# Optimization experiments

Measured on AMD Instinct MI355X. Metric: run time of the kernel, lower is better.

The kernel has to match this reference:

```python
import jax, jax.numpy as jnp
import numpy as np

V, D, H, B, S, T, N_EXTRA = 32000, 256, 512, 16, 400, 100, 50


def _lstm_cell(x, h, c, Wih, Whh, b):
    g = x @ Wih.T + h @ Whh.T + b
    i, f, gg, o = jnp.split(g, 4, axis=-1)
    c = jax.nn.sigmoid(f) * c + jax.nn.sigmoid(i) * jnp.tanh(gg)
    h = jax.nn.sigmoid(o) * jnp.tanh(c)
    return h, c


def _run_lstm(xs, m, Wih, Whh, b):
    # xs: [S,B,D], m: [S,B,1] validity mask (packed-sequence semantics)
    Bz, Hh = xs.shape[1], Whh.shape[1]
    init = (jnp.zeros((Bz, Hh), xs.dtype), jnp.zeros((Bz, Hh), xs.dtype))
    def step(carry, inp):
        h, c = carry
        x, mm = inp
        hn, cn = _lstm_cell(x, h, c, Wih, Whh, b)
        h = jnp.where(mm, hn, h)
        c = jnp.where(mm, cn, c)
        return (h, c), jnp.where(mm, hn, 0.0)
    (h, c), ys = jax.lax.scan(step, init, (xs, m))
    return ys, h, c


def setup_inputs():
    key = jax.random.key(0)
    ks = jax.random.split(key, 20)
    def gn(k, shape, scale=0.05):
        return jax.random.normal(k, shape, dtype=jnp.float32) * scale
    inp = {}
    inp["source"] = jax.random.randint(ks[0], (B, S), 0, V)
    inp["source_extended"] = jax.random.randint(ks[1], (B, S), 0, V + N_EXTRA)
    inp["source_length"] = jax.random.randint(ks[2], (B,), S // 2, S + 1)
    inp["target"] = jax.random.randint(ks[3], (B, T), 0, V)
    inp["emb"] = gn(ks[4], (V, D), 0.1)
    inp["enc_Wih_f"] = gn(ks[5], (4 * H, D))
    inp["enc_Whh_f"] = gn(ks[6], (4 * H, H))
    inp["enc_b_f"] = jnp.zeros((4 * H,), jnp.float32)
    inp["enc_Wih_b"] = gn(ks[7], (4 * H, D))
    inp["enc_Whh_b"] = gn(ks[8], (4 * H, H))
    inp["enc_b_b"] = jnp.zeros((4 * H,), jnp.float32)
    inp["Wproj"] = gn(ks[9], (H, 2 * H))
    inp["bproj"] = jnp.zeros((H,), jnp.float32)
    inp["W2h"] = gn(ks[10], (H, 2 * H))
    inp["b2h"] = jnp.zeros((H,), jnp.float32)
    inp["W2c"] = gn(ks[11], (H, 2 * H))
    inp["b2c"] = jnp.zeros((H,), jnp.float32)
    inp["Wo1"] = gn(ks[12], (H, 2 * H))
    inp["bo1"] = jnp.zeros((H,), jnp.float32)
    inp["Wo2"] = gn(ks[13], (D, H))
    inp["dec_Wih"] = gn(ks[14], (4 * H, 2 * D))
    inp["dec_Whh"] = gn(ks[15], (4 * H, H))
    inp["dec_b"] = jnp.zeros((4 * H,), jnp.float32)
    inp["Wpgen"] = gn(ks[16], (1, 2 * H + 2 * D))
    inp["bpgen"] = jnp.zeros((1,), jnp.float32)
    return inp


def reference(source, source_extended, source_length, target, emb,
              enc_Wih_f, enc_Whh_f, enc_b_f, enc_Wih_b, enc_Whh_b, enc_b_b,
              Wproj, bproj, W2h, b2h, W2c, b2c, Wo1, bo1, Wo2,
              dec_Wih, dec_Whh, dec_b, Wpgen, bpgen):
    mask = jnp.arange(S)[None, :] < source_length[:, None]  # [B,S]
    w_s = emb[source]                                        # [B,S,D]
    xs = jnp.swapaxes(w_s, 0, 1)                             # [S,B,D]
    m = jnp.swapaxes(mask, 0, 1)[:, :, None]                 # [S,B,1]
    # bidirectional LSTM encoder
    ys_f, h_f, c_f = _run_lstm(xs, m, enc_Wih_f, enc_Whh_f, enc_b_f)
    ys_b, h_b, c_b = _run_lstm(xs[::-1], m[::-1], enc_Wih_b, enc_Whh_b, enc_b_b)
    ys_b = ys_b[::-1]
    enc_outs = jnp.swapaxes(jnp.concatenate([ys_f, ys_b], -1), 0, 1)  # [B,S,2H]
    enc_outs = enc_outs @ Wproj.T + bproj                             # [B,S,H]
    dec_h = jnp.concatenate([h_f, h_b], -1) @ W2h.T + b2h             # [B,H]
    dec_c = jnp.concatenate([c_f, c_b], -1) @ W2c.T + b2c             # [B,H]
    lens = source_length[:, None].astype(enc_outs.dtype)
    seq_mean = (enc_outs * mask[..., None]).sum(1) / lens             # [B,H]
    def out_proj(x):
        return jnp.tanh(x @ Wo1.T + bo1) @ Wo2.T
    dec_out0 = out_proj(jnp.concatenate([dec_h, seq_mean], -1))       # [B,D]
    neg = jnp.finfo(enc_outs.dtype).min
    extra = jnp.zeros((B, N_EXTRA), enc_outs.dtype)
    rows = jnp.arange(B)[:, None]
    w_t = jnp.swapaxes(emb[target], 0, 1)                             # [T,B,D]
    def step(carry, x_t):
        dec_out, h, c = carry
        x = jnp.concatenate([x_t, dec_out], -1)                       # [B,2D]
        h, c = _lstm_cell(x, h, c, dec_Wih, dec_Whh, dec_b)
        scores = jnp.einsum('bh,bsh->bs', h, enc_outs)
        attn = jax.nn.softmax(jnp.where(mask, scores, neg), axis=-1)  # point_dist
        context = jnp.einsum('bs,bsh->bh', attn, enc_outs)
        p_gen = jax.nn.sigmoid(jnp.concatenate([context, h, x], -1) @ Wpgen.T + bpgen)  # [B,1]
        dec_out = out_proj(jnp.concatenate([h, context], -1))         # [B,D]
        logit = dec_out @ emb.T                                       # [B,V]
        vocab_dist = jnp.concatenate([p_gen * jax.nn.softmax(logit, axis=-1), extra], -1)
        final = vocab_dist.at[rows, source_extended].add((1.0 - p_gen) * attn) + 1e-20
        return (dec_out, h, c), jnp.log(final)
    _, logits = jax.lax.scan(step, (dec_out0, dec_h, dec_c), w_t)
    return logits  # [T,B,V+N_EXTRA]
```

## Files before the change

### kernel.cpp

```cpp
#include <hip/hip_runtime.h>

#define V_SZ 32000
#define D_SZ 256
#define H_SZ 512
#define B_SZ 16
#define S_SZ 400
#define T_SZ 100
#define G4   2048
#define VX   32050
#define LINE 32

typedef unsigned short ushort_t;
typedef __attribute__((ext_vector_type(8))) __bf16 bf16x8;
typedef __attribute__((ext_vector_type(8))) unsigned short ushort8_t;
typedef __attribute__((ext_vector_type(4))) float f32x4;

__device__ __forceinline__ ushort_t f2bf(float x) {
  union { float f; unsigned u; } v; v.f = x;
  unsigned r = v.u + 0x7fffu + ((v.u >> 16) & 1u);
  return (ushort_t)(r >> 16);
}
__device__ __forceinline__ float bf2f(ushort_t x) {
  union { unsigned u; float f; } v; v.u = ((unsigned)x) << 16; return v.f;
}
__device__ __forceinline__ float bfu2f(unsigned x) {
  union { unsigned u; float f; } v; v.u = x << 16; return v.f;
}
__device__ __forceinline__ float sigf(float x) { return 1.0f / (1.0f + __expf(-x)); }
__device__ __forceinline__ float tanh_f(float x) {
  float e = __expf(2.0f * x);
  return 1.0f - 2.0f / (e + 1.0f);
}
__device__ __forceinline__ float dot4(f32x4 a, f32x4 b) {
  return a.x * b.x + a.y * b.y + a.z * b.z + a.w * b.w;
}
__device__ __forceinline__ void stg(float* p, float v) {
  __hip_atomic_store(p, v, __ATOMIC_RELAXED, __HIP_MEMORY_SCOPE_AGENT);
}
__device__ __forceinline__ void stg_u32(unsigned* p, unsigned v) {
  __hip_atomic_store(p, v, __ATOMIC_RELAXED, __HIP_MEMORY_SCOPE_AGENT);
}

__device__ __forceinline__ void slot_barrier(unsigned* slots, int myslot, int nslots,
                                             unsigned pc) {
  asm volatile("s_waitcnt vmcnt(0)" ::: "memory");
  __syncthreads();
  if (threadIdx.x == 0)
    __hip_atomic_store(&slots[myslot * LINE], pc, __ATOMIC_RELAXED, __HIP_MEMORY_SCOPE_AGENT);
  if (threadIdx.x < 64) {
    const int i0 = threadIdx.x, i1 = threadIdx.x + 64;
    for (;;) {
      unsigned v0 = pc, v1 = pc;
      if (i0 < nslots)
        v0 = __hip_atomic_load(&slots[i0 * LINE], __ATOMIC_RELAXED, __HIP_MEMORY_SCOPE_AGENT);
      if (i1 < nslots)
        v1 = __hip_atomic_load(&slots[i1 * LINE], __ATOMIC_RELAXED, __HIP_MEMORY_SCOPE_AGENT);
      if (__all((v0 >= pc) & (v1 >= pc))) break;
      __builtin_amdgcn_s_sleep(1);
    }
  }
  __syncthreads();
}

__global__ __launch_bounds__(256) void cvt_kernel(const float* in, ushort_t* outp, int n) {
  int i = blockIdx.x * 256 + threadIdx.x;
  int stride = gridDim.x * 256;
  for (; i < n; i += stride) outp[i] = f2bf(in[i]);
}

__global__ __launch_bounds__(256) void cvt_strided_kernel(const float* in, ushort_t* outp) {
  int gid = blockIdx.x * 256 + threadIdx.x;
  int r = gid >> 8, d = gid & 255;
  outp[gid] = f2bf(in[(size_t)r * 512 + d]);
}

__global__ __launch_bounds__(256) void cvt_wo2t_kernel(const float* wo2, ushort_t* outp) {
  int gid = blockIdx.x * 256 + threadIdx.x;
  int h = gid >> 8, d = gid & 255;
  outp[gid] = f2bf(wo2[(size_t)d * 512 + h]);
}

__global__ __launch_bounds__(256) void wfused_kernel(const float* dwih, const float* wo2,
                                                     float* wf) {
  __shared__ float xr_s[256];
  int r = blockIdx.x;
  xr_s[threadIdx.x] = dwih[(size_t)r * 512 + 256 + threadIdx.x];
  __syncthreads();
  float a0 = 0, a1 = 0;
  for (int d = 0; d < 256; ++d) {
    float x = xr_s[d];
    a0 += x * wo2[(size_t)d * 512 + threadIdx.x];
    a1 += x * wo2[(size_t)d * 512 + threadIdx.x + 256];
  }
  wf[(size_t)r * 512 + threadIdx.x] = a0;
  wf[(size_t)r * 512 + threadIdx.x + 256] = a1;
}

__global__ __launch_bounds__(256) void wfp_kernel(const float* wpgen, const float* wo2,
                                                  float* wfp) {
  int h = blockIdx.x * 256 + threadIdx.x;
  float a = 0;
  for (int d = 0; d < 256; ++d) a += wpgen[1280 + d] * wo2[(size_t)d * 512 + h];
  wfp[h] = a;
}

__global__ __launch_bounds__(256) void pack_whh_kernel(const float* whh_f, const float* whh_b,
                                                       ushort_t* outp) {
  int gid = blockIdx.x * 256 + threadIdx.x;
  int col = gid & 511;
  int p_g = gid >> 9;
  int dir = p_g >> 11, p = p_g & 2047;
  int ub = p >> 6, g = (p >> 4) & 3, u = p & 15;
  const float* src = dir ? whh_b : whh_f;
  outp[gid] = f2bf(src[(size_t)(g * 512 + ub * 16 + u) * 512 + col]);
}
// ... 85 lines not shown
  mfma_16x64(ys_cat, wproj_bf, 2 * H_SZ, m0, n0, acc);
  int lane = threadIdx.x & 63, lr = lane & 15, kh = lane >> 4;
#pragma unroll
  for (int s = 0; s < 4; ++s) {
    int n = n0 + s * 16 + lr;
    float bv = bproj[n];
#pragma unroll
    for (int i = 0; i < 4; ++i) {
      int m = m0 + kh * 4 + i;
      int b = m & 15, si = m >> 4;
      enc_outs[((size_t)b * S_SZ + si) * H_SZ + n] = acc[s][i] + bv;
    }
  }
}

__global__ __launch_bounds__(256) void gemm_e2(const ushort_t* emb_bf, const ushort_t* wo2t_bf,
                                               ushort_t* e2) {
  int wave = threadIdx.x >> 6;
  int m0 = blockIdx.y * 16;
  int n0 = blockIdx.x * 256 + wave * 64;
  f32x4 acc[4] = {};
  mfma_16x64(emb_bf, wo2t_bf, 256, m0, n0, acc);
  int lane = threadIdx.x & 63, lr = lane & 15, kh = lane >> 4;
#pragma unroll
  for (int s = 0; s < 4; ++s) {
    int n = n0 + s * 16 + lr;
#pragma unroll
    for (int i = 0; i < 4; ++i) {
      int m = m0 + kh * 4 + i;
      e2[(size_t)m * 512 + n] = f2bf(acc[s][i]);
    }
  }
}

__global__ __launch_bounds__(256) void gemm_logits(const ushort_t* tmp_bf, const ushort_t* e2_bf,
                                                   float* out) {
  int wave = threadIdx.x >> 6;
  int m0 = blockIdx.x * 16;
  int n0 = blockIdx.y * 256 + wave * 64;
  f32x4 acc[4] = {};
  mfma_16x64(tmp_bf, e2_bf, 512, m0, n0, acc);
  int lane = threadIdx.x & 63, lr = lane & 15, kh = lane >> 4;
#pragma unroll
  for (int s = 0; s < 4; ++s) {
    int n = n0 + s * 16 + lr;
#pragma unroll
    for (int i = 0; i < 4; ++i) {
      int m = m0 + kh * 4 + i;
      out[(size_t)m * VX + n] = acc[s][i];
    }
  }
}

__global__ __launch_bounds__(256) void enc_kernel(const float* gx_f, const float* gx_b,
                                                  const ushort_t* whh_pk, const int* src_len,
                                                  unsigned* hbf_f, unsigned* hbf_b,
                                                  unsigned* ys_cat_u32, float* h_final,
                                                  float* c_final, unsigned* ctrs) {
  __shared__ float gates_s[4 * 16 * 17];
  const int blk = blockIdx.x, tid = threadIdx.x;
  const int dir = blk >> 5, ub = blk & 31, j0 = ub * 16;
  const int g = tid >> 6, lane = tid & 63, lr = lane & 15, kh = lane >> 4;
  const float* gx = dir ? gx_b : gx_f;
  unsigned* hb = dir ? hbf_b : hbf_f;
  unsigned* slots = ctrs + dir * 1024;
  const ushort_t* wrow =
      whh_pk + (size_t)(((dir * 32 + ub) * 4 + g) * 16 + lr) * 512 + kh * 8;
  const int bc = tid >> 4, uc = tid & 15;
  const int len_b = src_len[bc];
  float c_reg = 0.0f, h_reg = 0.0f;

  int maxlen;
  {
    int v = src_len[lane & 15];
    v = max(v, __shfl_xor(v, 1));
    v = max(v, __shfl_xor(v, 2));
    v = max(v, __shfl_xor(v, 4));
    v = max(v, __shfl_xor(v, 8));
    maxlen = v;
  }
  for (int i = tid; i < (S_SZ - maxlen) * 128; i += 256) {
    int s = maxlen + (i >> 7);
    int r = i & 127;
    int bb = r >> 3, k = r & 7;
    ys_cat_u32[(size_t)(s * 16 + bb) * 512 + dir * 256 + (j0 >> 1) + k] = 0u;
  }

  float gxa[4];
  {
    const int s0 = dir ? (maxlen - 1) : 0;
    const float* g0 = gx + (size_t)s0 * (16 * 2048) + g * 512 + j0 + lr;
#pragma unroll
    for (int i = 0; i < 4; ++i) gxa[i] = g0[(size_t)(kh * 4 + i) * 2048];
  }

  for (int t = 0; t < maxlen; ++t) {
    const int s_pos = dir ? (maxlen - 1 - t) : t;
    float gxn[4] = {0.f, 0.f, 0.f, 0.f};
    if (t + 1 < maxlen) {
      const int sn = dir ? (maxlen - 2 - t) : (t + 1);
      const float* gn = gx + (size_t)sn * (16 * 2048) + g * 512 + j0 + lr;
#pragma unroll
      for (int i = 0; i < 4; ++i) gxn[i] = gn[(size_t)(kh * 4 + i) * 2048];
    }
    f32x4 acc = {0.f, 0.f, 0.f, 0.f};
    const ushort_t* ap = (const ushort_t*)(hb + (size_t)t * 4096) + lr * 512 + kh * 8;
#pragma unroll
    for (int k0 = 0; k0 < 512; k0 += 32)
      acc = __builtin_amdgcn_mfma_f32_16x16x32_bf16(*(const bf16x8*)(ap + k0),
                                                    *(const bf16x8*)(wrow + k0), acc, 0, 0, 0);
#pragma unroll
    for (int i = 0; i < 4; ++i)
      gates_s[(g * 16 + lr) * 17 + kh * 4 + i] = acc[i] + gxa[i];
    __syncthreads();
    float gi = gates_s[uc * 17 + bc];
    float gf = gates_s[(16 + uc) * 17 + bc];
    float gg = gates_s[(32 + uc) * 17 + bc];
    float go = gates_s[(48 + uc) * 17 + bc];
    bool msk = s_pos < len_b;
    float cn = sigf(gf) * c_reg + sigf(gi) * tanh_f(gg);
    float hn = sigf(go) * tanh_f(cn);
    float hout = msk ? hn : h_reg;
    if (msk) c_reg = cn;
    h_reg = hout;
    unsigned hbits = (unsigned)f2bf(hout);
    unsigned hpart = __shfl_xor(hbits, 1);
    unsigned ybits = msk ? (unsigned)f2bf(hn) : 0u;
    unsigned ypart = __shfl_xor(ybits, 1);
    if ((uc & 1) == 0) {
      stg_u32(&hb[(size_t)(t + 1) * 4096 + bc * 256 + ((j0 + uc) >> 1)], hbits | (hpart << 16));
      ys_cat_u32[(size_t)(s_pos * 16 + bc) * 512 + dir * 256 + ((j0 + uc) >> 1)] =
          ybits | (ypart << 16);
    }
    if (t == maxlen - 1) {
      h_final[dir * 8192 + bc * 512 + j0 + uc] = hout;
      c_final[dir * 8192 + bc * 512 + j0 + uc] = c_reg;
    }
    if (t + 1 < maxlen) slot_barrier(slots, ub, 32, (unsigned)(t + 1));
#pragma unroll
    for (int i = 0; i < 4; ++i) gxa[i] = gxn[i];
  }
}

__global__ __launch_bounds__(256) void seqmean_kernel(const float* enc_outs, const int* src_len,
                                                      float* seq_mean) {
  int b = blockIdx.x >> 1;
  int j = (blockIdx.x & 1) * 256 + threadIdx.x;
  int L = src_len[b];
  float a = 0;
  for (int s = 0; s < L; ++s) a += enc_outs[((size_t)b * S_SZ + s) * H_SZ + j];
  seq_mean[b * 512 + j] = a / (float)L;
}

__global__ __launch_bounds__(256) void init_state_kernel(const float* h_final, const float* c_final,
                                                         const float* w2h, const float* b2h,
                                                         const float* w2c, const float* b2c,
                                                         unsigned* h_u32, float* c_init) {
  int gid = blockIdx.x * 256 + threadIdx.x;
  int half = gid >> 13;
  int idx = gid & 8191;
  int b = idx >> 9, j = idx & 511;
  const float* src = half ? c_final : h_final;
  const float* w = (half ? w2c : w2h) + (size_t)j * 1024;
  float acc = (half ? b2c : b2h)[j];
  const f32x4* s0 = (const f32x4*)(src + b * 512);
  const f32x4* s1 = (const f32x4*)(src + 8192 + b * 512);
  const f32x4* w0 = (const f32x4*)w;
  const f32x4* w1 = w0 + 128;
  float a = 0;
  for (int k = 0; k < 128; ++k) a += dot4(s0[k], w0[k]);
  for (int k = 0; k < 128; ++k) a += dot4(s1[k], w1[k]);
  acc += a;
  if (half) {
    c_init[idx] = acc;
  } else {
    unsigned bits = (unsigned)f2bf(acc);
    unsigned pb2 = __shfl_xor(bits, 1);
    if ((j & 1) == 0) h_u32[b * 256 + (j >> 1)] = bits | (pb2 << 16);
  }
}

__global__ __launch_bounds__(256) void tmp0_kernel(const unsigned* h0_u32, const float* seq_mean,
                                                   const float* wo1, const float* bo1,
                                                   unsigned* tmp_u32) {
  int gid = blockIdx.x * 256 + threadIdx.x;
  int b = gid >> 9, j = gid & 511;
  const f32x4* x1 = (const f32x4*)(seq_mean + b * 512);
  const f32x4* w0 = (const f32x4*)(wo1 + (size_t)j * 1024);
  const f32x4* w1 = w0 + 128;
  float a = bo1[j];
  float p = 0;
  const ushort_t* h0 = (const ushort_t*)(h0_u32) + b * 512;
  for (int k = 0; k < 128; ++k) {
    f32x4 hv = {bf2f(h0[k * 4]), bf2f(h0[k * 4 + 1]), bf2f(h0[k * 4 + 2]), bf2f(h0[k * 4 + 3])};
    p += dot4(hv, w0[k]);
  }
  for (int k = 0; k < 128; ++k) p += dot4(x1[k], w1[k]);
  float tv = tanh_f(a + p);
  unsigned bits = (unsigned)f2bf(tv);
  unsigned pb2 = __shfl_xor(bits, 1);
  if ((j & 1) == 0) tmp_u32[b * 256 + (j >> 1)] = bits | (pb2 << 16);
}

__global__ __launch_bounds__(256) void dec_kernel(
    const ushort_t* xt_bf, const int* src_len, const ushort_t* wdec_pk,
    const float* wpgen, const float* bpgen, const float* wfp, const ushort_t* wo1_bf,
    const float* bo1, const float* enc_outs, const float* gxT, unsigned* h_u32,
    const float* c_init, unsigned* tmp_u32, float* ctx_part, float* z_part, float* zinv,
    float* pgen_o, float* pexp, unsigned* ctrs) {
  __shared__ ushort_t ec_s[50 * 512];
  __shared__ float part_s[4 * 16 * 17];
  __shared__ f32x4 smem4[272];
  __shared__ float red_s[8];
  __shared__ float p_s[64];
  float* sm = (float*)smem4;
  unsigned* gslots = ctrs + 2048;

  const int blk = blockIdx.x, tid = threadIdx.x;
  const int w = tid >> 6, lane = tid & 63, lr = lane & 15, kh = lane >> 4;
  const int j0 = blk * 4;
  const ushort_t* wrow = wdec_pk + (size_t)(blk * 16 + lr) * 1024 + w * 256 + kh * 8;
  const int b_c = (tid >> 2) & 15, u_c = tid & 3;
  float c_reg = (tid < 64) ? c_init[b_c * 512 + j0 + u_c] : 0.0f;
  const int b_pb = blk >> 3, ch = blk & 7, s0c = ch * 50;
  const int len_pb = src_len[b_pb];
  const int nc = ch;
  unsigned* grslots = ctrs + 8192 + b_pb * 256;
  unsigned gpc = 0;

  {
    const f32x4* ebase = (const f32x4*)(enc_outs + ((size_t)b_pb * S_SZ + s0c) * H_SZ);
    unsigned* dst = (unsigned*)ec_s;
    for (int i = tid; i < 6400; i += 256) {
      f32x4 v = ebase[i];
      dst[2 * i] = (unsigned)f2bf(v.x) | ((unsigned)f2bf(v.y) << 16);
      dst[2 * i + 1] = (unsigned)f2bf(v.z) | ((unsigned)f2bf(v.w) << 16);
    }
  }

  float gxa[4] = {0.f, 0.f, 0.f, 0.f};
  if (tid < 64) {
#pragma unroll
    for (int g2 = 0; g2 < 4; ++g2)
      gxa[g2] = gxT[((size_t)(g2 * 512 + j0 + u_c)) * 16 + b_c];
  }

  for (int t = 0; t < T_SZ; ++t) {
    {
      f32x4 acc = {0.f, 0.f, 0.f, 0.f};
      const unsigned* asrc = (w < 2) ? (h_u32 + (size_t)t * 4096) : (tmp_u32 + (size_t)t * 4096);
      const ushort_t* ap = (const ushort_t*)asrc + lr * 512 + (w & 1) * 256 + kh * 8;
#pragma unroll
      for (int k0 = 0; k0 < 256; k0 += 32)
        acc = __builtin_amdgcn_mfma_f32_16x16x32_bf16(*(const bf16x8*)(ap + k0),
                                                      *(const bf16x8*)(wrow + k0), acc, 0, 0, 0);
#pragma unroll
      for (int i = 0; i < 4; ++i) part_s[(w * 16 + lr) * 17 + kh * 4 + i] = acc[i];
      __syncthreads();
      if (tid < 64) {
        float gt[4];
#pragma unroll
        for (int g2 = 0; g2 < 4; ++g2) {
          int p = g2 * 4 + u_c;
          float a = gxa[g2];
#pragma unroll
          for (int w2 = 0; w2 < 4; ++w2) a += part_s[(w2 * 16 + p) * 17 + b_c];
          gt[g2] = a;
        }
        float cn = sigf(gt[1]) * c_reg + sigf(gt[0]) * tanh_f(gt[2]);
        c_reg = cn;
        float hn = sigf(gt[3]) * tanh_f(cn);
        unsigned bits = (unsigned)f2bf(hn);
        unsigned pb2 = __shfl_xor(bits, 1);
        if ((u_c & 1) == 0)
          stg_u32(&h_u32[(size_t)(t + 1) * 4096 + b_c * 256 + ((j0 + u_c) >> 1)],
                  bits | (pb2 << 16));
      }
    }
    slot_barrier(gslots, blk, 128, ++gpc);
    {
      if (tid < 64 && t + 1 < T_SZ) {
#pragma unroll
        for (int g2 = 0; g2 < 4; ++g2)
          gxa[g2] = gxT[((size_t)(t + 1) * G4 + g2 * 512 + j0 + u_c) * 16 + b_c];
      }
      if (tid < 128) {
        unsigned v0 = h_u32[(size_t)(t + 1) * 4096 + b_pb * 256 + tid * 2];
        unsigned v1 = h_u32[(size_t)(t + 1) * 4096 + b_pb * 256 + tid * 2 + 1];
        f32x4 hv = {bfu2f(v0 & 0xffffu), bfu2f(v0 >> 16), bfu2f(v1 & 0xffffu), bfu2f(v1 >> 16)};
        ((f32x4*)sm)[tid] = hv;
      }
      __syncthreads();
      int st = tid >> 2, kq = tid & 3;
      if (st < 50) {
        const ushort8_t* er = (const ushort8_t*)(ec_s + st * 512) + kq * 16;
        const f32x4* hr = (const f32x4*)sm + kq * 32;
        float sc = 0;
#pragma unroll 4
        for (int k = 0; k < 16; ++k) {
          ushort8_t w8 = er[k];
          f32x4 w0 = {bf2f(w8[0]), bf2f(w8[1]), bf2f(w8[2]), bf2f(w8[3])};
          f32x4 w1 = {bf2f(w8[4]), bf2f(w8[5]), bf2f(w8[6]), bf2f(w8[7])};
          sc += dot4(hr[2 * k], w0) + dot4(hr[2 * k + 1], w1);
        }
        sc += __shfl_xor(sc, 1);
        sc += __shfl_xor(sc, 2);
        if (kq == 0) {
          int s_abs = s0c + st;
          float p = (s_abs < len_pb) ? __expf(sc) : 0.0f;
          p_s[st] = p;
          pexp[((size_t)t * 16 + b_pb) * S_SZ + s_abs] = p;
        }
      }
      __syncthreads();
      if (tid == 0) {
        float z = 0;
        for (int s = 0; s < 50; ++s) z += p_s[s];
        stg(&z_part[((size_t)t * 16 + b_pb) * 8 + ch], z);
      }
      float a0 = 0, a1 = 0;
      for (int s = 0; s < 50; ++s) {
        float p = p_s[s];
        a0 += p * bf2f(ec_s[s * 512 + tid]);
        a1 += p * bf2f(ec_s[s * 512 + tid + 256]);
      }
      float* cp = ctx_part + (((size_t)t * 16 + b_pb) * 8 + ch) * 512;
      stg(&cp[tid], a0);
      stg(&cp[tid + 256], a1);
    }
    slot_barrier(grslots, ch, 8, (unsigned)(t + 1));
    {
      float* h_s = sm;
      float* ctx_s = sm + 512;
      const float* zp = z_part + ((size_t)t * 16 + b_pb) * 8;
      float z = 0;
#pragma unroll
      for (int c2 = 0; c2 < 8; ++c2) z += zp[c2];
      float inv = 1.0f / z;
      const float* cpb = ctx_part + ((size_t)t * 16 + b_pb) * 8 * 512;
      float c0 = 0, c1 = 0;
#pragma unroll
      for (int c2 = 0; c2 < 8; ++c2) {
        c0 += cpb[c2 * 512 + tid];
        c1 += cpb[c2 * 512 + tid + 256];
      }
      ctx_s[tid] = c0 * inv;
      ctx_s[tid + 256] = c1 * inv;
      __syncthreads();
      const ushort_t* tmpp = (const ushort_t*)(tmp_u32 + (size_t)t * 4096) + b_pb * 512;
      float tp0 = bf2f(tmpp[tid]);
      float tp1 = bf2f(tmpp[tid + 256]);
      float xe = bf2f(xt_bf[((size_t)t * 16 + b_pb) * 256 + tid]);
      float pg = wpgen[tid] * ctx_s[tid] + wpgen[tid + 256] * ctx_s[tid + 256] +
                 wpgen[512 + tid] * h_s[tid] + wpgen[512 + tid + 256] * h_s[tid + 256] +
                 wpgen[1024 + tid] * xe + wfp[tid] * tp0 + wfp[tid + 256] * tp1;
#pragma unroll
      for (int o = 32; o; o >>= 1) pg += __shfl_xor(pg, o);
      if (lane == 0) red_s[w] = pg;
      __syncthreads();
      if (nc == 0 && tid == 0) {
        pgen_o[t * 16 + b_pb] = sigf(red_s[0] + red_s[1] + red_s[2] + red_s[3] + bpgen[0]);
        zinv[t * 16 + b_pb] = inv;
      }
      int nidx = tid >> 2, kq = tid & 3;
      int n = nc * 64 + nidx;
      const ushort8_t* wrp = (const ushort8_t*)(wo1_bf + (size_t)n * 1024) + kq * 32;
      const f32x4* xr2 =
          (kq < 2) ? ((const f32x4*)h_s + kq * 64) : ((const f32x4*)ctx_s + (kq - 2) * 64);
      float a = 0;
#pragma unroll 4
      for (int k = 0; k < 32; ++k) {
        ushort8_t w8 = wrp[k];
        f32x4 w0 = {bf2f(w8[0]), bf2f(w8[1]), bf2f(w8[2]), bf2f(w8[3])};
        f32x4 w1 = {bf2f(w8[4]), bf2f(w8[5]), bf2f(w8[6]), bf2f(w8[7])};
        a += dot4(xr2[2 * k], w0) + dot4(xr2[2 * k + 1], w1);
      }
      a += __shfl_xor(a, 1);
      a += __shfl_xor(a, 2);
      float tv = tanh_f(a + bo1[n]);
      unsigned bits = (unsigned)f2bf(tv);
      unsigned pbits = __shfl_xor(bits, 4);
      if (kq == 0 && (nidx & 1) == 0)
        stg_u32(&tmp_u32[(size_t)(t + 1) * 4096 + b_pb * 256 + ((nc * 64 + nidx) >> 1)],
                bits | (pbits << 16));
    }
    if (t + 1 < T_SZ) slot_barrier(gslots, blk, 128, ++gpc);
  }
}

__global__ __launch_bounds__(1024) void finalize_kernel(float* out, const float* pexp,
                                                        const float* zinv, const float* pgen_i,
                                                        const int* src_ext) {
  __shared__ float scat[VX];
  __shared__ float red[64];
  const int row = blockIdx.x;
  const int b = row & 15;
  const int tid = threadIdx.x;
  for (int i = tid; i < VX; i += 1024) scat[i] = 0.0f;
  __syncthreads();
  const float pg = pgen_i[row];
  const float inv = zinv[row];
  if (tid < S_SZ) {
    float v = (1.0f - pg) * pexp[(size_t)row * S_SZ + tid] * inv;
    int col = src_ext[b * S_SZ + tid];
    atomicAdd(&scat[col], v);
  }
  float* orow = out + (size_t)row * VX;
  float l[32];
  float mx = -3.4e38f;
#pragma unroll
  for (int i2 = 0; i2 < 32; ++i2) {
    int col = tid + (i2 << 10);
    l[i2] = (col < V_SZ) ? orow[col] : -3.4e38f;
    mx = fmaxf(mx, l[i2]);
  }
#pragma unroll
  for (int o = 32; o; o >>= 1) mx = fmaxf(mx, __shfl_xor(mx, o));
  if ((tid & 63) == 0) red[16 + (tid >> 6)] = mx;
  __syncthreads();
  if (tid == 0) {
    float m2 = red[16];
    for (int w = 1; w < 16; ++w) m2 = fmaxf(m2, red[16 + w]);
    red[0] = m2;
  }
  __syncthreads();
  const float gmx = red[0];
  float se = 0.0f;
#pragma unroll
  for (int i2 = 0; i2 < 32; ++i2) {
    int col = tid + (i2 << 10);
    if (col < V_SZ) {
      l[i2] = __expf(l[i2] - gmx);
      se += l[i2];
    }
  }
#pragma unroll
  for (int o = 32; o; o >>= 1) se += __shfl_xor(se, o);
  if ((tid & 63) == 0) red[32 + (tid >> 6)] = se;
  __syncthreads();
// ... 1 lines not shown
    float s2 = 0;
    for (int w = 0; w < 16; ++w) s2 += red[32 + w];
    red[1] = s2;
  }
  __syncthreads();
  const float scale = pg / red[1];
#pragma unroll
  for (int i2 = 0; i2 < 32; ++i2) {
    int col = tid + (i2 << 10);
    if (col < VX) {
      float base = (col < V_SZ) ? l[i2] * scale : 0.0f;
      orow[col] = __logf(base + scat[col] + 1e-20f);
    }
  }
}

extern "C" void kernel_launch(void* const* d_in, const int* in_sizes, int n_in, void* d_out,
                              int out_size, void* d_ws, size_t ws_size, hipStream_t stream) {
  (void)in_sizes; (void)n_in; (void)out_size; (void)ws_size;
  const int* source = (const int*)d_in[0];
  const int* source_ext = (const int*)d_in[1];
  const int* source_len = (const int*)d_in[2];
  const int* target = (const int*)d_in[3];
  const float* emb = (const float*)d_in[4];
  const float* wih_f = (const float*)d_in[5];
  const float* whh_f = (const float*)d_in[6];
  const float* b_f = (const float*)d_in[7];
  const float* wih_b = (const float*)d_in[8];
  const float* whh_b = (const float*)d_in[9];
  const float* b_b = (const float*)d_in[10];
  const float* wproj = (const float*)d_in[11];
  const float* bproj = (const float*)d_in[12];
  const float* w2h = (const float*)d_in[13];
  const float* b2h = (const float*)d_in[14];
  const float* w2c = (const float*)d_in[15];
  const float* b2c = (const float*)d_in[16];
  const float* wo1 = (const float*)d_in[17];
  const float* bo1 = (const float*)d_in[18];
  const float* wo2 = (const float*)d_in[19];
  const float* dwih = (const float*)d_in[20];
  const float* dwhh = (const float*)d_in[21];
  const float* dbias = (const float*)d_in[22];
  const float* wpgen = (const float*)d_in[23];
  const float* bpgen = (const float*)d_in[24];
  float* out = (float*)d_out;

  size_t off = 0;
  char* wsb = (char*)d_ws;
  auto alloc = [&](size_t bytes) -> void* {
    void* p = wsb + off;
    off += (bytes + 255) & ~(size_t)255;
    return p;
  };
  unsigned* ctrs = (unsigned*)alloc(64 * 1024);
  ushort_t* emb_bf = (ushort_t*)alloc((size_t)V_SZ * D_SZ * 2);
  ushort_t* wihf_bf = (ushort_t*)alloc((size_t)G4 * D_SZ * 2);
  ushort_t* wihb_bf = (ushort_t*)alloc((size_t)G4 * D_SZ * 2);
  ushort_t* wihd_bf = (ushort_t*)alloc((size_t)G4 * D_SZ * 2);
  ushort_t* wproj_bf = (ushort_t*)alloc((size_t)H_SZ * 2 * H_SZ * 2);
  ushort_t* wo2t_bf = (ushort_t*)alloc((size_t)H_SZ * D_SZ * 2);
  ushort_t* wo1_bf = (ushort_t*)alloc((size_t)H_SZ * 1024 * 2);
  float* wfused = (float*)alloc((size_t)G4 * H_SZ * 4);
  float* wfp = (float*)alloc(512 * 4);
  ushort_t* whh_pk = (ushort_t*)alloc((size_t)2 * G4 * H_SZ * 2);
  ushort_t* wdec_pk = (ushort_t*)alloc((size_t)G4 * 1024 * 2);
  ushort_t* xs_bf = (ushort_t*)alloc((size_t)S_SZ * B_SZ * D_SZ * 2);
  ushort_t* xt_bf = (ushort_t*)alloc((size_t)T_SZ * B_SZ * D_SZ * 2);
  float* gx_f = (float*)alloc((size_t)S_SZ * B_SZ * G4 * 4);
  float* gx_b = (float*)alloc((size_t)S_SZ * B_SZ * G4 * 4);
  unsigned* hbf_f = (unsigned*)alloc((size_t)(S_SZ + 1) * 4096 * 4);
  unsigned* hbf_b = (unsigned*)alloc((size_t)(S_SZ + 1) * 4096 * 4);
  unsigned* ys_cat_u32 = (unsigned*)alloc((size_t)S_SZ * B_SZ * 512 * 4);
  float* h_final = (float*)alloc((size_t)2 * B_SZ * H_SZ * 4);
  float* c_final = (float*)alloc((size_t)2 * B_SZ * H_SZ * 4);
  float* enc_outs = (float*)alloc((size_t)B_SZ * S_SZ * H_SZ * 4);
  float* seq_mean = (float*)alloc((size_t)B_SZ * H_SZ * 4);
  unsigned* h_u32 = (unsigned*)alloc((size_t)(T_SZ + 1) * 4096 * 4);
  float* c_init = (float*)alloc((size_t)B_SZ * H_SZ * 4);
  unsigned* tmp_u32 = (unsigned*)alloc((size_t)(T_SZ + 1) * 4096 * 4);
  float* z_part = (float*)alloc((size_t)T_SZ * B_SZ * 8 * 4);
  float* zinv = (float*)alloc((size_t)T_SZ * B_SZ * 4);
  float* pgen_b = (float*)alloc((size_t)T_SZ * B_SZ * 4);
  float* pexp = (float*)alloc((size_t)T_SZ * B_SZ * S_SZ * 4);
  ushort_t* e2_bf = (ushort_t*)gx_f;
  float* gx_dec = gx_b;
  float* ctx_part = gx_b + (size_t)3276800;
  float* gxT = gx_b + (size_t)9830400;

  hipMemsetAsync(ctrs, 0, 64 * 1024, stream);
  hipMemsetAsync(hbf_f, 0, 4096 * 4, stream);
  hipMemsetAsync(hbf_b, 0, 4096 * 4, stream);

  cvt_kernel<<<2048, 256, 0, stream>>>(emb, emb_bf, V_SZ * D_SZ);
  cvt_kernel<<<2048, 256, 0, stream>>>(wih_f, wihf_bf, G4 * D_SZ);
  cvt_kernel<<<2048, 256, 0, stream>>>(wih_b, wihb_bf, G4 * D_SZ);
  cvt_kernel<<<2048, 256, 0, stream>>>(wproj, wproj_bf, H_SZ * 2 * H_SZ);
  cvt_kernel<<<2048, 256, 0, stream>>>(wo1, wo1_bf, H_SZ * 1024);
  cvt_strided_kernel<<<2048, 256, 0, stream>>>(dwih, wihd_bf);
  cvt_wo2t_kernel<<<512, 256, 0, stream>>>(wo2, wo2t_bf);
  wfused_kernel<<<2048, 256, 0, stream>>>(dwih, wo2, wfused);
  wfp_kernel<<<2, 256, 0, stream>>>(wpgen, wo2, wfp);
  pack_whh_kernel<<<8192, 256, 0, stream>>>(whh_f, whh_b, whh_pk);
  pack_wdec_kernel<<<8192, 256, 0, stream>>>(dwhh, wfused, wdec_pk);
  gather_src_kernel<<<800, 256, 0, stream>>>(emb_bf, source, xs_bf);
  gather_tgt_kernel<<<200, 256, 0, stream>>>(emb_bf, target, xt_bf);
  gemm_abt_bias<<<dim3(8, 400), 256, 0, stream>>>(xs_bf, wihf_bf, b_f, gx_f, 256);
  gemm_abt_bias<<<dim3(8, 400), 256, 0, stream>>>(xs_bf, wihb_bf, b_b, gx_b, 256);
  enc_kernel<<<64, 256, 0, stream>>>(gx_f, gx_b, whh_pk, source_len, hbf_f, hbf_b, ys_cat_u32,
                                     h_final, c_final, ctrs);
  gemm_encout<<<dim3(2, 400), 256, 0, stream>>>((const ushort_t*)ys_cat_u32, wproj_bf, bproj,
                                                enc_outs);
  seqmean_kernel<<<32, 256, 0, stream>>>(enc_outs, source_len, seq_mean);
  init_state_kernel<<<64, 256, 0, stream>>>(h_final, c_final, w2h, b2h, w2c, b2c, h_u32, c_init);
  tmp0_kernel<<<32, 256, 0, stream>>>(h_u32, seq_mean, wo1, bo1, tmp_u32);
  gemm_abt_bias<<<dim3(8, 100), 256, 0, stream>>>(xt_bf, wihd_bf, dbias, gx_dec, 256);
  gxT_kernel<<<dim3(8, 100), 256, 0, stream>>>(gx_dec, gxT);
  gemm_e2<<<dim3(2, 2000), 256, 0, stream>>>(emb_bf, wo2t_bf, e2_bf);
  dec_kernel<<<128, 256, 0, stream>>>(xt_bf, source_len, wdec_pk, wpgen, bpgen, wfp, wo1_bf, bo1,
                                      enc_outs, gxT, h_u32, c_init, tmp_u32, ctx_part, z_part,
                                      zinv, pgen_b, pexp, ctrs);
  gemm_logits<<<dim3(100, 125), 256, 0, stream>>>((const ushort_t*)(tmp_u32 + 4096), e2_bf, out);
  finalize_kernel<<<1600, 1024, 0, stream>>>(out, pexp, zinv, pgen_b, source_ext);
}
```

Before: 4.863 ms.

## Replace counter-slot grid barriers with sentinel-valued data polling in recurrent kernels

```diff
diff --git a/kernel.cpp b/kernel.cpp
--- a/kernel.cpp
+++ b/kernel.cpp
@@ -8,7 +8,7 @@
 #define T_SZ 100
 #define G4   2048
 #define VX   32050
-#define LINE 32
+#define SENTU 0xFFFFFFFFu
 
 typedef unsigned short ushort_t;
 typedef __attribute__((ext_vector_type(8))) __bf16 bf16x8;
@@ -26,6 +26,9 @@
 __device__ __forceinline__ float bfu2f(unsigned x) {
   union { unsigned u; float f; } v; v.u = x << 16; return v.f;
 }
+__device__ __forceinline__ float u2f(unsigned x) {
+  union { unsigned u; float f; } v; v.u = x; return v.f;
+}
 __device__ __forceinline__ float sigf(float x) { return 1.0f / (1.0f + __expf(-x)); }
 __device__ __forceinline__ float tanh_f(float x) {
   float e = __expf(2.0f * x);
@@ -40,27 +43,11 @@
 __device__ __forceinline__ void stg_u32(unsigned* p, unsigned v) {
   __hip_atomic_store(p, v, __ATOMIC_RELAXED, __HIP_MEMORY_SCOPE_AGENT);
 }
-
-__device__ __forceinline__ void slot_barrier(unsigned* slots, int myslot, int nslots,
-                                             unsigned pc) {
-  asm volatile("s_waitcnt vmcnt(0)" ::: "memory");
-  __syncthreads();
-  if (threadIdx.x == 0)
-    __hip_atomic_store(&slots[myslot * LINE], pc, __ATOMIC_RELAXED, __HIP_MEMORY_SCOPE_AGENT);
-  if (threadIdx.x < 64) {
-    const int i0 = threadIdx.x, i1 = threadIdx.x + 64;
-    for (;;) {
-      unsigned v0 = pc, v1 = pc;
-      if (i0 < nslots)
-        v0 = __hip_atomic_load(&slots[i0 * LINE], __ATOMIC_RELAXED, __HIP_MEMORY_SCOPE_AGENT);
-      if (i1 < nslots)
-        v1 = __hip_atomic_load(&slots[i1 * LINE], __ATOMIC_RELAXED, __HIP_MEMORY_SCOPE_AGENT);
-      if (__all((v0 >= pc) & (v1 >= pc))) break;
-      __builtin_amdgcn_s_sleep(1);
-    }
-  }
-  __syncthreads();
-}
+__device__ __forceinline__ unsigned pollu(const unsigned* p) {
+  return __hip_atomic_load(p, __ATOMIC_RELAXED, __HIP_MEMORY_SCOPE_AGENT);
+}
+
+union U8 { unsigned u[4]; bf16x8 v; };
 
 __global__ __launch_bounds__(256) void cvt_kernel(const float* in, ushort_t* outp, int n) {
   int i = blockIdx.x * 256 + threadIdx.x;
@@ -256,19 +243,22 @@
                                                   const ushort_t* whh_pk, const int* src_len,
                                                   unsigned* hbf_f, unsigned* hbf_b,
                                                   unsigned* ys_cat_u32, float* h_final,
-                                                  float* c_final, unsigned* ctrs) {
+                                                  float* c_final) {
   __shared__ float gates_s[4 * 16 * 17];
   const int blk = blockIdx.x, tid = threadIdx.x;
   const int dir = blk >> 5, ub = blk & 31, j0 = ub * 16;
   const int g = tid >> 6, lane = tid & 63, lr = lane & 15, kh = lane >> 4;
   const float* gx = dir ? gx_b : gx_f;
   unsigned* hb = dir ? hbf_b : hbf_f;
-  unsigned* slots = ctrs + dir * 1024;
   const ushort_t* wrow =
       whh_pk + (size_t)(((dir * 32 + ub) * 4 + g) * 16 + lr) * 512 + kh * 8;
   const int bc = tid >> 4, uc = tid & 15;
   const int len_b = src_len[bc];
   float c_reg = 0.0f, h_reg = 0.0f;
+
+  bf16x8 wv[16];
+#pragma unroll
+  for (int k = 0; k < 16; ++k) wv[k] = *(const bf16x8*)(wrow + k * 32);
 
   int maxlen;
   {
@@ -303,12 +293,33 @@
 #pragma unroll
       for (int i = 0; i < 4; ++i) gxn[i] = gn[(size_t)(kh * 4 + i) * 2048];
     }
+    U8 hv[16];
+    if (t == 0) {
+#pragma unroll
+      for (int k = 0; k < 16; ++k) {
+        hv[k].u[0] = 0; hv[k].u[1] = 0; hv[k].u[2] = 0; hv[k].u[3] = 0;
+      }
+    } else {
+      const unsigned* hp = hb + (size_t)t * 4096 + lr * 256 + kh * 4;
+      for (;;) {
+        unsigned okm = 1u;
+#pragma unroll
+        for (int k = 0; k < 16; ++k) {
+#pragma unroll
+          for (int q = 0; q < 4; ++q) {
+            unsigned v = pollu(&hp[k * 16 + q]);
+            hv[k].u[q] = v;
+            okm &= (v != SENTU) ? 1u : 0u;
+          }
+        }
+        if (__all((int)okm)) break;
+        __builtin_amdgcn_s_sleep(1);
+      }
+    }
     f32x4 acc = {0.f, 0.f, 0.f, 0.f};
-    const ushort_t* ap = (const ushort_t*)(hb + (size_t)t * 4096) + lr * 512 + kh * 8;
-#pragma unroll
-    for (int k0 = 0; k0 < 512; k0 += 32)
-      acc = __builtin_amdgcn_mfma_f32_16x16x32_bf16(*(const bf16x8*)(ap + k0),
-                                                    *(const bf16x8*)(wrow + k0), acc, 0, 0, 0);
+#pragma unroll
+    for (int k = 0; k < 16; ++k)
+      acc = __builtin_amdgcn_mfma_f32_16x16x32_bf16(hv[k].v, wv[k], acc, 0, 0, 0);
 #pragma unroll
     for (int i = 0; i < 4; ++i)
       gates_s[(g * 16 + lr) * 17 + kh * 4 + i] = acc[i] + gxa[i];
@@ -336,7 +347,7 @@
       h_final[dir * 8192 + bc * 512 + j0 + uc] = hout;
       c_final[dir * 8192 + bc * 512 + j0 + uc] = c_reg;
     }
-    if (t + 1 < maxlen) slot_barrier(slots, ub, 32, (unsigned)(t + 1));
+    __syncthreads();
 #pragma unroll
     for (int i = 0; i < 4; ++i) gxa[i] = gxn[i];
   }
@@ -407,14 +418,13 @@
     const float* wpgen, const float* bpgen, const float* wfp, const ushort_t* wo1_bf,
     const float* bo1, const float* enc_outs, const float* gxT, unsigned* h_u32,
     const float* c_init, unsigned* tmp_u32, float* ctx_part, float* z_part, float* zinv,
-    float* pgen_o, float* pexp, unsigned* ctrs) {
+    float* pgen_o, float* pexp) {
   __shared__ ushort_t ec_s[50 * 512];
   __shared__ float part_s[4 * 16 * 17];
   __shared__ f32x4 smem4[272];
   __shared__ float red_s[8];
   __shared__ float p_s[64];
   float* sm = (float*)smem4;
-  unsigned* gslots = ctrs + 2048;
 
   const int blk = blockIdx.x, tid = threadIdx.x;
   const int w = tid >> 6, lane = tid & 63, lr = lane & 15, kh = lane >> 4;
@@ -425,8 +435,10 @@
   const int b_pb = blk >> 3, ch = blk & 7, s0c = ch * 50;
   const int len_pb = src_len[b_pb];
   const int nc = ch;
-  unsigned* grslots = ctrs + 8192 + b_pb * 256;
-  unsigned gpc = 0;
+
+  bf16x8 wv[8];
+#pragma unroll
+  for (int k = 0; k < 8; ++k) wv[k] = *(const bf16x8*)(wrow + k * 32);
 
   {
     const f32x4* ebase = (const f32x4*)(enc_outs + ((size_t)b_pb * S_SZ + s0c) * H_SZ);
@@ -447,13 +459,27 @@
 
   for (int t = 0; t < T_SZ; ++t) {
     {
+      const unsigned* asrc = (w < 2) ? (h_u32 + (size_t)t * 4096) : (tmp_u32 + (size_t)t * 4096);
+      const unsigned* hp = asrc + lr * 256 + (w & 1) * 128 + kh * 4;
+      U8 hv[8];
+      for (;;) {
+        unsigned okm = 1u;
+#pragma unroll
+        for (int k = 0; k < 8; ++k) {
+#pragma unroll
+          for (int q = 0; q < 4; ++q) {
+            unsigned v = pollu(&hp[k * 16 + q]);
+            hv[k].u[q] = v;
+            okm &= (v != SENTU) ? 1u : 0u;
+          }
+        }
+        if (__all((int)okm)) break;
+        __builtin_amdgcn_s_sleep(1);
+      }
       f32x4 acc = {0.f, 0.f, 0.f, 0.f};
-      const unsigned* asrc = (w < 2) ? (h_u32 + (size_t)t * 4096) : (tmp_u32 + (size_t)t * 4096);
-      const ushort_t* ap = (const ushort_t*)asrc + lr * 512 + (w & 1) * 256 + kh * 8;
-#pragma unroll
-      for (int k0 = 0; k0 < 256; k0 += 32)
-        acc = __builtin_amdgcn_mfma_f32_16x16x32_bf16(*(const bf16x8*)(ap + k0),
-                                                      *(const bf16x8*)(wrow + k0), acc, 0, 0, 0);
+#pragma unroll
+      for (int k = 0; k < 8; ++k)
+        acc = __builtin_amdgcn_mfma_f32_16x16x32_bf16(hv[k].v, wv[k], acc, 0, 0, 0);
 #pragma unroll
       for (int i = 0; i < 4; ++i) part_s[(w * 16 + lr) * 17 + kh * 4 + i] = acc[i];
       __syncthreads();
@@ -476,8 +502,8 @@
           stg_u32(&h_u32[(size_t)(t + 1) * 4096 + b_c * 256 + ((j0 + u_c) >> 1)],
                   bits | (pb2 << 16));
       }
-    }
-    slot_barrier(gslots, blk, 128, ++gpc);
+      __syncthreads();
+    }
     {
       if (tid < 64 && t + 1 < T_SZ) {
 #pragma unroll
@@ -485,8 +511,14 @@
           gxa[g2] = gxT[((size_t)(t + 1) * G4 + g2 * 512 + j0 + u_c) * 16 + b_c];
       }
       if (tid < 128) {
-        unsigned v0 = h_u32[(size_t)(t + 1) * 4096 + b_pb * 256 + tid * 2];
-        unsigned v1 = h_u32[(size_t)(t + 1) * 4096 + b_pb * 256 + tid * 2 + 1];
+        const unsigned* hp = h_u32 + (size_t)(t + 1) * 4096 + b_pb * 256 + tid * 2;
+        unsigned v0, v1;
+        for (;;) {
+          v0 = pollu(hp);
+          v1 = pollu(hp + 1);
+          if (__all((v0 != SENTU) & (v1 != SENTU))) break;
+          __builtin_amdgcn_s_sleep(1);
+        }
         f32x4 hv = {bfu2f(v0 & 0xffffu), bfu2f(v0 >> 16), bfu2f(v1 & 0xffffu), bfu2f(v1 >> 16)};
         ((f32x4*)sm)[tid] = hv;
       }
@@ -528,28 +560,46 @@
       stg(&cp[tid], a0);
       stg(&cp[tid + 256], a1);
     }
-    slot_barrier(grslots, ch, 8, (unsigned)(t + 1));
     {
       float* h_s = sm;
       float* ctx_s = sm + 512;
-      const float* zp = z_part + ((size_t)t * 16 + b_pb) * 8;
+      const unsigned* zpu = (const unsigned*)(z_part + ((size_t)t * 16 + b_pb) * 8);
+      const unsigned* cpu = (const unsigned*)(ctx_part + ((size_t)t * 16 + b_pb) * 8 * 512);
+      const unsigned* tpu = tmp_u32 + (size_t)t * 4096 + b_pb * 256;
+      unsigned zv[8], cva[8], cvb[8], tva, tvb;
+      for (;;) {
+        unsigned okm = 1u;
+#pragma unroll
+        for (int c2 = 0; c2 < 8; ++c2) {
+          zv[c2] = pollu(&zpu[c2]);
+          okm &= (zv[c2] != SENTU) ? 1u : 0u;
+          cva[c2] = pollu(&cpu[c2 * 512 + tid]);
+          okm &= (cva[c2] != SENTU) ? 1u : 0u;
+          cvb[c2] = pollu(&cpu[c2 * 512 + tid + 256]);
+          okm &= (cvb[c2] != SENTU) ? 1u : 0u;
+        }
+        tva = pollu(&tpu[tid >> 1]);
+        okm &= (tva != SENTU) ? 1u : 0u;
+        tvb = pollu(&tpu[128 + (tid >> 1)]);
+        okm &= (tvb != SENTU) ? 1u : 0u;
+        if (__all((int)okm)) break;
+        __builtin_amdgcn_s_sleep(1);
+      }
       float z = 0;
 #pragma unroll
-      for (int c2 = 0; c2 < 8; ++c2) z += zp[c2];
+      for (int c2 = 0; c2 < 8; ++c2) z += u2f(zv[c2]);
       float inv = 1.0f / z;
-      const float* cpb = ctx_part + ((size_t)t * 16 + b_pb) * 8 * 512;
       float c0 = 0, c1 = 0;
 #pragma unroll
       for (int c2 = 0; c2 < 8; ++c2) {
-        c0 += cpb[c2 * 512 + tid];
-        c1 += cpb[c2 * 512 + tid + 256];
+        c0 += u2f(cva[c2]);
+        c1 += u2f(cvb[c2]);
       }
       ctx_s[tid] = c0 * inv;
       ctx_s[tid + 256] = c1 * inv;
       __syncthreads();
-      const ushort_t* tmpp = (const ushort_t*)(tmp_u32 + (size_t)t * 4096) + b_pb * 512;
-      float tp0 = bf2f(tmpp[tid]);
-      float tp1 = bf2f(tmpp[tid + 256]);
+      float tp0 = bf2f((ushort_t)((tid & 1) ? (tva >> 16) : (tva & 0xffffu)));
+      float tp1 = bf2f((ushort_t)((tid & 1) ? (tvb >> 16) : (tvb & 0xffffu)));
       float xe = bf2f(xt_bf[((size_t)t * 16 + b_pb) * 256 + tid]);
       float pg = wpgen[tid] * ctx_s[tid] + wpgen[tid + 256] * ctx_s[tid + 256] +
                  wpgen[512 + tid] * h_s[tid] + wpgen[512 + tid + 256] * h_s[tid + 256] +
@@ -583,8 +633,8 @@
       if (kq == 0 && (nidx & 1) == 0)
         stg_u32(&tmp_u32[(size_t)(t + 1) * 4096 + b_pb * 256 + ((nc * 64 + nidx) >> 1)],
                 bits | (pbits << 16));
-    }
-    if (t + 1 < T_SZ) slot_barrier(gslots, blk, 128, ++gpc);
+      __syncthreads();
+    }
   }
 }
 
@@ -692,7 +742,6 @@
     off += (bytes + 255) & ~(size_t)255;
     return p;
   };
-  unsigned* ctrs = (unsigned*)alloc(64 * 1024);
   ushort_t* emb_bf = (ushort_t*)alloc((size_t)V_SZ * D_SZ * 2);
   ushort_t* wihf_bf = (ushort_t*)alloc((size_t)G4 * D_SZ * 2);
   ushort_t* wihb_bf = (ushort_t*)alloc((size_t)G4 * D_SZ * 2);
@@ -727,9 +776,11 @@
   float* ctx_part = gx_b + (size_t)3276800;
   float* gxT = gx_b + (size_t)9830400;
 
-  hipMemsetAsync(ctrs, 0, 64 * 1024, stream);
-  hipMemsetAsync(hbf_f, 0, 4096 * 4, stream);
-  hipMemsetAsync(hbf_b, 0, 4096 * 4, stream);
+  hipMemsetAsync(hbf_f, 0xFF, (size_t)(S_SZ + 1) * 4096 * 4, stream);
+  hipMemsetAsync(hbf_b, 0xFF, (size_t)(S_SZ + 1) * 4096 * 4, stream);
+  hipMemsetAsync(h_u32, 0xFF, (size_t)(T_SZ + 1) * 4096 * 4, stream);
+  hipMemsetAsync(tmp_u32, 0xFF, (size_t)(T_SZ + 1) * 4096 * 4, stream);
+  hipMemsetAsync(z_part, 0xFF, (size_t)T_SZ * B_SZ * 8 * 4, stream);
 
   cvt_kernel<<<2048, 256, 0, stream>>>(emb, emb_bf, V_SZ * D_SZ);
   cvt_kernel<<<2048, 256, 0, stream>>>(wih_f, wihf_bf, G4 * D_SZ);
@@ -747,7 +798,7 @@
   gemm_abt_bias<<<dim3(8, 400), 256, 0, stream>>>(xs_bf, wihf_bf, b_f, gx_f, 256);
   gemm_abt_bias<<<dim3(8, 400), 256, 0, stream>>>(xs_bf, wihb_bf, b_b, gx_b, 256);
   enc_kernel<<<64, 256, 0, stream>>>(gx_f, gx_b, whh_pk, source_len, hbf_f, hbf_b, ys_cat_u32,
-                                     h_final, c_final, ctrs);
+                                     h_final, c_final);
   gemm_encout<<<dim3(2, 400), 256, 0, stream>>>((const ushort_t*)ys_cat_u32, wproj_bf, bproj,
                                                 enc_outs);
   seqmean_kernel<<<32, 256, 0, stream>>>(enc_outs, source_len, seq_mean);
@@ -756,9 +807,10 @@
   gemm_abt_bias<<<dim3(8, 100), 256, 0, stream>>>(xt_bf, wihd_bf, dbias, gx_dec, 256);
   gxT_kernel<<<dim3(8, 100), 256, 0, stream>>>(gx_dec, gxT);
   gemm_e2<<<dim3(2, 2000), 256, 0, stream>>>(emb_bf, wo2t_bf, e2_bf);
+  hipMemsetAsync(ctx_part, 0xFF, (size_t)T_SZ * B_SZ * 8 * H_SZ * 4, stream);
   dec_kernel<<<128, 256, 0, stream>>>(xt_bf, source_len, wdec_pk, wpgen, bpgen, wfp, wo1_bf, bo1,
                                       enc_outs, gxT, h_u32, c_init, tmp_u32, ctx_part, z_part,
-                                      zinv, pgen_b, pexp, ctrs);
+                                      zinv, pgen_b, pexp);
   gemm_logits<<<dim3(100, 125), 256, 0, stream>>>((const ushort_t*)(tmp_u32 + 4096), e2_bf, out);
   finalize_kernel<<<1600, 1024, 0, stream>>>(out, pexp, zinv, pgen_b, source_ext);
 }
```

Result: slower. 7.452 ms (+53.2%).

## Pin encoder LSTM blocks to one XCC per direction and sync via local L2

Applied to the files above, without the earlier changes.

```diff
diff --git a/kernel.cpp b/kernel.cpp
--- a/kernel.cpp
+++ b/kernel.cpp
@@ -39,6 +39,20 @@
 }
 __device__ __forceinline__ void stg_u32(unsigned* p, unsigned v) {
   __hip_atomic_store(p, v, __ATOMIC_RELAXED, __HIP_MEMORY_SCOPE_AGENT);
+}
+__device__ __forceinline__ unsigned pollu(const unsigned* p) {
+  return __hip_atomic_load(p, __ATOMIC_RELAXED, __HIP_MEMORY_SCOPE_AGENT);
+}
+__device__ __forceinline__ unsigned ld_sc0(const unsigned* p) {
+  unsigned v;
+  asm volatile("global_load_dword %0, %1, off sc0\n\ts_waitcnt vmcnt(0)"
+               : "=&v"(v) : "v"(p) : "memory");
+  return v;
+}
+__device__ __forceinline__ int xcc_id() {
+  unsigned v;
+  asm volatile("s_getreg_b32 %0, hwreg(HW_REG_XCC_ID)" : "=s"(v));
+  return (int)(v & 0xf);
 }
 
 __device__ __forceinline__ void slot_barrier(unsigned* slots, int myslot, int nslots,
@@ -252,23 +266,45 @@
   }
 }
 
-__global__ __launch_bounds__(256) void enc_kernel(const float* gx_f, const float* gx_b,
-                                                  const ushort_t* whh_pk, const int* src_len,
-                                                  unsigned* hbf_f, unsigned* hbf_b,
-                                                  unsigned* ys_cat_u32, float* h_final,
-                                                  float* c_final, unsigned* ctrs) {
-  __shared__ float gates_s[4 * 16 * 17];
-  const int blk = blockIdx.x, tid = threadIdx.x;
-  const int dir = blk >> 5, ub = blk & 31, j0 = ub * 16;
+__global__ __launch_bounds__(256, 1) void enc_kernel(const float* gx_f, const float* gx_b,
+                                                     const ushort_t* whh_pk, const int* src_len,
+                                                     unsigned* hb_f, unsigned* hb_b,
+                                                     unsigned* hbM_f, unsigned* hbM_b,
+                                                     unsigned* ys_cat_u32, float* h_final,
+                                                     float* c_final, unsigned* ctrs) {
+  __shared__ float big_s[25600];
+  __shared__ int role_s;
+  __shared__ int ok_s;
+  float* gates_s = big_s;
+  const int tid = threadIdx.x;
+  if (tid == 0) {
+    int xcc = xcc_id();
+    int r = -1;
+    if (xcc == 0) {
+      unsigned i = atomicAdd(&ctrs[12288], 1u);
+      if (i < 32u) r = (int)i;
+    } else if (xcc == 1) {
+      unsigned i = atomicAdd(&ctrs[12320], 1u);
+      if (i < 32u) r = 32 + (int)i;
+    }
+    role_s = r;
+  }
+  __syncthreads();
+  const int role = role_s;
+  if (role < 0) return;
+  const int dir = role >> 5, ub = role & 31, j0 = ub * 16;
   const int g = tid >> 6, lane = tid & 63, lr = lane & 15, kh = lane >> 4;
   const float* gx = dir ? gx_b : gx_f;
-  unsigned* hb = dir ? hbf_b : hbf_f;
-  unsigned* slots = ctrs + dir * 1024;
+  unsigned* hb = dir ? hb_b : hb_f;
+  unsigned* hbM = dir ? hbM_b : hbM_f;
+  unsigned* tl = ctrs + dir * 1024;
+  unsigned* tm = ctrs + 2048 + dir * 1024;
   const ushort_t* wrow =
       whh_pk + (size_t)(((dir * 32 + ub) * 4 + g) * 16 + lr) * 512 + kh * 8;
   const int bc = tid >> 4, uc = tid & 15;
   const int len_b = src_len[bc];
   float c_reg = 0.0f, h_reg = 0.0f;
+  bool slow = false;
 
   int maxlen;
   {
@@ -281,8 +317,8 @@
   }
   for (int i = tid; i < (S_SZ - maxlen) * 128; i += 256) {
     int s = maxlen + (i >> 7);
-    int r = i & 127;
-    int bb = r >> 3, k = r & 7;
+    int r2 = i & 127;
+    int bb = r2 >> 3, k = r2 & 7;
     ys_cat_u32[(size_t)(s * 16 + bb) * 512 + dir * 256 + (j0 >> 1) + k] = 0u;
   }
 
@@ -303,8 +339,34 @@
 #pragma unroll
       for (int i = 0; i < 4; ++i) gxn[i] = gn[(size_t)(kh * 4 + i) * 2048];
     }
+    const unsigned* hsrcbuf = hb;
+    if (t > 0) {
+      if (tid < 64) {
+        int ok = 0;
+        if (!slow) {
+          for (int it = 0; it < 2000; ++it) {
+            unsigned v = (unsigned)t;
+            if (lane < 32) v = ld_sc0(&tl[lane * 32]);
+            if (__all((int)(v >= (unsigned)t))) { ok = 1; break; }
+            __builtin_amdgcn_s_sleep(1);
+          }
+        }
+        if (!ok) {
+          for (;;) {
+            unsigned v = (unsigned)t;
+            if (lane < 32) v = pollu(&tm[lane * 32]);
+            if (__all((int)(v >= (unsigned)t))) break;
+            __builtin_amdgcn_s_sleep(1);
+          }
+        }
+        if (tid == 0) ok_s = ok;
+      }
+      __syncthreads();
+      if (!ok_s) slow = true;
+      hsrcbuf = ok_s ? hb : hbM;
+    }
     f32x4 acc = {0.f, 0.f, 0.f, 0.f};
-    const ushort_t* ap = (const ushort_t*)(hb + (size_t)t * 4096) + lr * 512 + kh * 8;
+    const ushort_t* ap = (const ushort_t*)(hsrcbuf + (size_t)t * 4096) + lr * 512 + kh * 8;
 #pragma unroll
     for (int k0 = 0; k0 < 512; k0 += 32)
       acc = __builtin_amdgcn_mfma_f32_16x16x32_bf16(*(const bf16x8*)(ap + k0),
@@ -328,7 +390,10 @@
     unsigned ybits = msk ? (unsigned)f2bf(hn) : 0u;
     unsigned ypart = __shfl_xor(ybits, 1);
     if ((uc & 1) == 0) {
-      stg_u32(&hb[(size_t)(t + 1) * 4096 + bc * 256 + ((j0 + uc) >> 1)], hbits | (hpart << 16));
+      unsigned wv2 = hbits | (hpart << 16);
+      size_t ix = (size_t)(t + 1) * 4096 + bc * 256 + ((j0 + uc) >> 1);
+      hb[ix] = wv2;
+      stg_u32(&hbM[ix], wv2);
       ys_cat_u32[(size_t)(s_pos * 16 + bc) * 512 + dir * 256 + ((j0 + uc) >> 1)] =
           ybits | (ypart << 16);
     }
@@ -336,7 +401,12 @@
       h_final[dir * 8192 + bc * 512 + j0 + uc] = hout;
       c_final[dir * 8192 + bc * 512 + j0 + uc] = c_reg;
     }
-    if (t + 1 < maxlen) slot_barrier(slots, ub, 32, (unsigned)(t + 1));
+    asm volatile("s_waitcnt vmcnt(0)" ::: "memory");
+    __syncthreads();
+    if (tid == 0) {
+      tl[ub * 32] = (unsigned)(t + 1);
+      stg_u32(&tm[ub * 32], (unsigned)(t + 1));
+    }
 #pragma unroll
     for (int i = 0; i < 4; ++i) gxa[i] = gxn[i];
   }
@@ -414,7 +484,7 @@
   __shared__ float red_s[8];
   __shared__ float p_s[64];
   float* sm = (float*)smem4;
-  unsigned* gslots = ctrs + 2048;
+  unsigned* gslots = ctrs + 4096;
 
   const int blk = blockIdx.x, tid = threadIdx.x;
   const int w = tid >> 6, lane = tid & 63, lr = lane & 15, kh = lane >> 4;
@@ -708,8 +778,10 @@
   ushort_t* xt_bf = (ushort_t*)alloc((size_t)T_SZ * B_SZ * D_SZ * 2);
   float* gx_f = (float*)alloc((size_t)S_SZ * B_SZ * G4 * 4);
   float* gx_b = (float*)alloc((size_t)S_SZ * B_SZ * G4 * 4);
-  unsigned* hbf_f = (unsigned*)alloc((size_t)(S_SZ + 1) * 4096 * 4);
-  unsigned* hbf_b = (unsigned*)alloc((size_t)(S_SZ + 1) * 4096 * 4);
+  unsigned* hb_f = (unsigned*)alloc((size_t)(S_SZ + 1) * 4096 * 4);
+  unsigned* hb_b = (unsigned*)alloc((size_t)(S_SZ + 1) * 4096 * 4);
+  unsigned* hbM_f = (unsigned*)alloc((size_t)(S_SZ + 1) * 4096 * 4);
+  unsigned* hbM_b = (unsigned*)alloc((size_t)(S_SZ + 1) * 4096 * 4);
   unsigned* ys_cat_u32 = (unsigned*)alloc((size_t)S_SZ * B_SZ * 512 * 4);
   float* h_final = (float*)alloc((size_t)2 * B_SZ * H_SZ * 4);
   float* c_final = (float*)alloc((size_t)2 * B_SZ * H_SZ * 4);
@@ -728,8 +800,10 @@
   float* gxT = gx_b + (size_t)9830400;
 
   hipMemsetAsync(ctrs, 0, 64 * 1024, stream);
-  hipMemsetAsync(hbf_f, 0, 4096 * 4, stream);
-  hipMemsetAsync(hbf_b, 0, 4096 * 4, stream);
+  hipMemsetAsync(hb_f, 0, 4096 * 4, stream);
+  hipMemsetAsync(hb_b, 0, 4096 * 4, stream);
+  hipMemsetAsync(hbM_f, 0, 4096 * 4, stream);
+  hipMemsetAsync(hbM_b, 0, 4096 * 4, stream);
 
   cvt_kernel<<<2048, 256, 0, stream>>>(emb, emb_bf, V_SZ * D_SZ);
   cvt_kernel<<<2048, 256, 0, stream>>>(wih_f, wihf_bf, G4 * D_SZ);
@@ -746,8 +820,8 @@
   gather_tgt_kernel<<<200, 256, 0, stream>>>(emb_bf, target, xt_bf);
   gemm_abt_bias<<<dim3(8, 400), 256, 0, stream>>>(xs_bf, wihf_bf, b_f, gx_f, 256);
   gemm_abt_bias<<<dim3(8, 400), 256, 0, stream>>>(xs_bf, wihb_bf, b_b, gx_b, 256);
-  enc_kernel<<<64, 256, 0, stream>>>(gx_f, gx_b, whh_pk, source_len, hbf_f, hbf_b, ys_cat_u32,
-                                     h_final, c_final, ctrs);
+  enc_kernel<<<256, 256, 0, stream>>>(gx_f, gx_b, whh_pk, source_len, hb_f, hb_b, hbM_f, hbM_b,
+                                      ys_cat_u32, h_final, c_final, ctrs);
   gemm_encout<<<dim3(2, 400), 256, 0, stream>>>((const ushort_t*)ys_cat_u32, wproj_bf, bproj,
                                                 enc_outs);
   seqmean_kernel<<<32, 256, 0, stream>>>(enc_outs, source_len, seq_mean);
```

Measured after the change: 5.045 ms. 3.7% more time.
